# Kernel tuning notes

Hardware: AMD Instinct MI355X
Metric: run time of the kernel (lower is better)

Reference implementation:

```python
import jax, jax.numpy as jnp
import numpy as np

BLOCK = 32
A16_QMAX = 32767.0  # symmetric 16-bit activation fake-quant
W4_QMAX = 7.0       # symmetric 4-bit per-block weight fake-quant (LPBQ)
EPS = 1e-12


def qdq_a16_per_tensor(x):
    # per-tensor symmetric 16-bit fake quantize / dequantize
    scale = jnp.maximum(jnp.max(jnp.abs(x)) / A16_QMAX, EPS)
    return jnp.clip(jnp.round(x / scale), -A16_QMAX - 1.0, A16_QMAX) * scale


def qdq_weight_lpbq(w):
    # w: [out, in]; block-size-32 groups along the input dim, int4 symmetric
    o, i = w.shape
    wb = w.reshape(o, i // BLOCK, BLOCK)
    scale = jnp.maximum(jnp.max(jnp.abs(wb), axis=-1, keepdims=True) / W4_QMAX, EPS)
    q = jnp.clip(jnp.round(wb / scale), -W4_QMAX - 1.0, W4_QMAX) * scale
    return q.reshape(o, i)


def setup_inputs() -> dict:
    key = jax.random.key(0)
    k0, k1, k2, k3 = jax.random.split(key, 4)
    T, H, I = 4096, 2048, 6144  # tokens, hidden, intermediate
    x = jax.random.normal(k0, (T, H), dtype=jnp.float32)
    w_gate = jax.random.normal(k1, (I, H), dtype=jnp.float32) * 0.02
    w_up = jax.random.normal(k2, (I, H), dtype=jnp.float32) * 0.02
    w_down = jax.random.normal(k3, (H, I), dtype=jnp.float32) * 0.02
    return {"x": x, "w_gate": w_gate, "w_up": w_up, "w_down": w_down}


def reference(x, w_gate, w_up, w_down):
    x = qdq_a16_per_tensor(x)
    up = qdq_a16_per_tensor(x @ qdq_weight_lpbq(w_up).T)      # [T, I]
    gate = qdq_a16_per_tensor(x @ qdq_weight_lpbq(w_gate).T)  # [T, I]
    act = qdq_a16_per_tensor(jax.nn.silu(up))                  # SiLU on up branch (as in source)
    mid = qdq_a16_per_tensor(gate * act)
    return mid @ qdq_weight_lpbq(w_down).T                     # [T, H]
```

## Files before the change

kernel.cpp:

```cpp
#include <hip/hip_runtime.h>

#define T_DIM 4096
#define H_DIM 2048
#define I_DIM 6144

#define BM 128
#define BN 128
#define BK 64

typedef __bf16 bf16x8 __attribute__((ext_vector_type(8)));
typedef float f32x4 __attribute__((ext_vector_type(4)));

__device__ __forceinline__ unsigned short f2bf(float f) {
  unsigned u = __float_as_uint(f);
  u += 0x7FFFu + ((u >> 16) & 1u);
  return (unsigned short)(u >> 16);
}
__device__ __forceinline__ float bf2f(unsigned short h) {
  return __uint_as_float(((unsigned)h) << 16);
}

__device__ __forceinline__ void async16(const unsigned short* g, unsigned short* l) {
  __builtin_amdgcn_global_load_lds(
      (__attribute__((address_space(1))) void*)g,
      (__attribute__((address_space(3))) void*)l, 16, 0, 0);
}

__device__ __forceinline__ void qdq_w_one(const float* __restrict__ w,
                                          unsigned short* __restrict__ out, int i) {
  float4 v = ((const float4*)w)[i];
  float m = fmaxf(fmaxf(fabsf(v.x), fabsf(v.y)), fmaxf(fabsf(v.z), fabsf(v.w)));
  m = fmaxf(m, __shfl_xor(m, 1));
  m = fmaxf(m, __shfl_xor(m, 2));
  m = fmaxf(m, __shfl_xor(m, 4));
  const float s = fmaxf(m * (1.0f / 7.0f), 1e-12f);
  const float inv = 1.0f / s;
  ushort4 o;
  o.x = f2bf(fminf(fmaxf(rintf(v.x * inv), -8.f), 7.f) * s);
  o.y = f2bf(fminf(fmaxf(rintf(v.y * inv), -8.f), 7.f) * s);
  o.z = f2bf(fminf(fmaxf(rintf(v.z * inv), -8.f), 7.f) * s);
  o.w = f2bf(fminf(fmaxf(rintf(v.w * inv), -8.f), 7.f) * s);
  ((ushort4*)out)[i] = o;
}

__global__ void k_prep(const float* __restrict__ x, unsigned short* __restrict__ xq,
                       const float* __restrict__ w0, unsigned short* __restrict__ o0,
                       const float* __restrict__ w1, unsigned short* __restrict__ o1,
                       const float* __restrict__ w2, unsigned short* __restrict__ o2,
                       int nx4, int nw4) {
  const int i = blockIdx.x * blockDim.x + threadIdx.x;
  if (i < nx4) {
    float4 v = ((const float4*)x)[i];
    ushort4 o;
    o.x = f2bf(v.x); o.y = f2bf(v.y); o.z = f2bf(v.z); o.w = f2bf(v.w);
    ((ushort4*)xq)[i] = o;
  } else if (i < nx4 + nw4) {
    qdq_w_one(w0, o0, i - nx4);
  } else if (i < nx4 + 2 * nw4) {
    qdq_w_one(w1, o1, i - nx4 - nw4);
  } else {
    qdq_w_one(w2, o2, i - nx4 - 2 * nw4);
  }
}

template <int LDK>
__device__ __forceinline__ void gemm_core(const unsigned short* __restrict__ A,
                                          const unsigned short* __restrict__ B,
                                          unsigned short* ldsA, unsigned short* ldsB,
                                          long m0, long n0, int tid, f32x4 acc[4][4]) {
  const int lane = tid & 63;
  const int wv = tid >> 6;
  const int wm = (wv >> 1) << 6;
  const int wn = (wv & 1) << 6;
  const int quad = lane >> 4;
  const int l16 = lane & 15;
  const int sw = (l16 & 7);

  for (int k0 = 0; k0 < LDK; k0 += BK) {
    __syncthreads();
#pragma unroll
    for (int r = 0; r < 4; ++r) {
      const int c = r * 256 + tid;
      const int row = c >> 3;
      const int colc = ((c & 7) ^ (row & 7)) * 8;
      async16(A + (m0 + row) * LDK + k0 + colc, ldsA + (size_t)c * 8);
      async16(B + (n0 + row) * LDK + k0 + colc, ldsB + (size_t)c * 8);
    }
    __syncthreads();

#pragma unroll
    for (int ks = 0; ks < BK / 32; ++ks) {
      bf16x8 af[4], bfr[4];
      const int sj = ((ks * 4 + quad) ^ sw) * 8;
#pragma unroll
      for (int i = 0; i < 4; ++i) {
        af[i] = *(const bf16x8*)(ldsA + (wm + i * 16 + l16) * BK + sj);
        bfr[i] = *(const bf16x8*)(ldsB + (wn + i * 16 + l16) * BK + sj);
      }
#pragma unroll
      for (int i = 0; i < 4; ++i)
#pragma unroll
        for (int j = 0; j < 4; ++j)
          acc[i][j] = __builtin_amdgcn_mfma_f32_16x16x32_bf16(af[i], bfr[j], acc[i][j], 0, 0, 0);
    }
  }
}

__launch_bounds__(512)
__global__ void k_gemm_ug_fused(const unsigned short* __restrict__ xq,
                                const unsigned short* __restrict__ wu,
                                const unsigned short* __restrict__ wg,
                                unsigned short* __restrict__ mid) {
  __shared__ unsigned short lds[3 * BM * BK];
  const int tid = threadIdx.x;
  const int lane = tid & 63;
  const int wv = tid >> 6;
  const int half = wv >> 2;
  const int wq = wv & 3;
  const int wm = (wq >> 1) << 6;
  const int wn = (wq & 1) << 6;
  const int quad = lane >> 4;
  const int l16 = lane & 15;
  const int sw = (l16 & 7);
  const long m0 = (long)blockIdx.y * BM;
  const long n0 = (long)blockIdx.x * BN;
  unsigned short* ldsB = lds + (size_t)(1 + half) * BM * BK;

  f32x4 acc[4][4] = {};

  for (int k0 = 0; k0 < H_DIM; k0 += BK) {
    __syncthreads();
#pragma unroll
    for (int r = 0; r < 6; ++r) {
      const int idx = r * 512 + tid;
      const int t = idx >> 10;
      const int c = idx & 1023;
      const int row = c >> 3;
      const int colc = ((c & 7) ^ (row & 7)) * 8;
      const unsigned short* src =
          (t == 0) ? xq + (m0 + row) * H_DIM + k0 + colc
        : (t == 1) ? wu + (n0 + row) * H_DIM + k0 + colc
                   : wg + (n0 + row) * H_DIM + k0 + colc;
      async16(src, lds + (size_t)t * (BM * BK) + (size_t)c * 8);
    }
    __syncthreads();

#pragma unroll
    for (int ks = 0; ks < BK / 32; ++ks) {
      bf16x8 af[4], bfr[4];
      const int sj = ((ks * 4 + quad) ^ sw) * 8;
#pragma unroll
      for (int i = 0; i < 4; ++i) {
        af[i] = *(const bf16x8*)(lds + (wm + i * 16 + l16) * BK + sj);
        bfr[i] = *(const bf16x8*)(ldsB + (wn + i * 16 + l16) * BK + sj);
      }
#pragma unroll
      for (int i = 0; i < 4; ++i)
#pragma unroll
        for (int j = 0; j < 4; ++j)
          acc[i][j] = __builtin_amdgcn_mfma_f32_16x16x32_bf16(af[i], bfr[j], acc[i][j], 0, 0, 0);
    }
  }

  __syncthreads();
  const int rbase = wm + (quad << 2);
  const int cbase = wn + l16;
  if (half) {
#pragma unroll
    for (int i = 0; i < 4; ++i)
#pragma unroll
      for (int r = 0; r < 4; ++r) {
        const int row = rbase + i * 16 + r;
        const int swz = ((row >> 2) & 3) << 4;
#pragma unroll
        for (int j = 0; j < 4; ++j) {
          const int col = cbase + j * 16;
          lds[row * 128 + (col ^ swz)] = f2bf(acc[i][j][r]);
        }
      }
  }
  __syncthreads();
  if (!half) {
#pragma unroll
    for (int i = 0; i < 4; ++i)
#pragma unroll
      for (int r = 0; r < 4; ++r) {
        const int row = rbase + i * 16 + r;
        const int swz = ((row >> 2) & 3) << 4;
        const long grow = m0 + row;
#pragma unroll
        for (int j = 0; j < 4; ++j) {
          const int col = cbase + j * 16;
          const float u = acc[i][j][r];
          const float g = bf2f(lds[row * 128 + (col ^ swz)]);
          const float a = u * __frcp_rn(1.0f + __expf(-u));
          mid[grow * (long)I_DIM + n0 + col] = f2bf(a * g);
        }
      }
  }
}

__launch_bounds__(256)
__global__ void k_gemm_down(const unsigned short* __restrict__ A,
                            const unsigned short* __restrict__ B,
                            float* __restrict__ C) {
  __shared__ unsigned short lds[(BM + BN) * BK];
  const int tid = threadIdx.x;
  const long m0 = (long)blockIdx.y * BM;
  const long n0 = (long)blockIdx.x * BN;

  f32x4 acc[4][4] = {};
  gemm_core<I_DIM>(A, B, lds, lds + BM * BK, m0, n0, tid, acc);

  const int lane = tid & 63;
  const int wv = tid >> 6;
  const int wm = (wv >> 1) << 6;
  const int wn = (wv & 1) << 6;
  const int quad = lane >> 4;
  const int l16 = lane & 15;
  const long rbase = m0 + wm + (quad << 2);
  const long cbase = n0 + wn + l16;
#pragma unroll
  for (int i = 0; i < 4; ++i)
#pragma unroll
    for (int r = 0; r < 4; ++r) {
      const long grow = rbase + i * 16 + r;
#pragma unroll
      for (int j = 0; j < 4; ++j)
        C[grow * (long)H_DIM + cbase + j * 16] = acc[i][j][r];
    }
}

extern "C" void kernel_launch(void* const* d_in, const int* in_sizes, int n_in,
                              void* d_out, int out_size, void* d_ws, size_t ws_size,
                              hipStream_t stream) {
  (void)in_sizes; (void)n_in; (void)out_size; (void)ws_size;
  const float* x      = (const float*)d_in[0];
  const float* w_gate = (const float*)d_in[1];
  const float* w_up   = (const float*)d_in[2];
  const float* w_down = (const float*)d_in[3];

  char* ws = (char*)d_ws;
  const size_t OFF_XQ = 0;
  const size_t OFF_WU = OFF_XQ + (size_t)T_DIM * H_DIM * 2;
  const size_t OFF_WD = OFF_WU + (size_t)I_DIM * H_DIM * 2;
  const size_t OFF_MID = OFF_WD + (size_t)I_DIM * H_DIM * 2;
  unsigned short* xq  = (unsigned short*)(ws + OFF_XQ);
  unsigned short* wuq = (unsigned short*)(ws + OFF_WU);
  unsigned short* wdq = (unsigned short*)(ws + OFF_WD);
  unsigned short* mid = (unsigned short*)(ws + OFF_MID);
  unsigned short* wgq = (unsigned short*)d_out;

  const int nx4 = T_DIM * H_DIM / 4;
  const int nw4 = I_DIM * H_DIM / 4;

  k_prep<<<(nx4 + 3 * nw4) / 256, 256, 0, stream>>>(x, xq, w_up, wuq, w_gate, wgq,
                                                    w_down, wdq, nx4, nw4);

  k_gemm_ug_fused<<<dim3(I_DIM / BN, T_DIM / BM), 512, 0, stream>>>(xq, wuq, wgq, mid);

  k_gemm_down<<<dim3(H_DIM / BN, T_DIM / BM), 256, 0, stream>>>(mid, wdq, (float*)d_out);
}
```

Measured before the change: 503.5 us.

## Double-buffer LDS in both GEMMs and widen down-proj tile to 128x256

Both the fused up/gate GEMM and the down-projection GEMM now use two LDS buffers. The async global-to-LDS load for the next K slice is issued before computing on the current one, which removes one barrier per iteration and overlaps memory traffic with MFMA work. The down GEMM also moves to 512 threads with a 128x256 tile, which raises reuse of the A operand and halves its grid. The cost is doubled LDS use: 96KB for the fused kernel and 96KB for the down kernel, which likely limits occupancy to one block per CU. The down GEMM grid drops to 256 blocks.

```diff
diff --git a/kernel.cpp b/kernel.cpp
--- a/kernel.cpp
+++ b/kernel.cpp
@@ -7,6 +7,7 @@
 #define BM 128
 #define BN 128
 #define BK 64
+#define DBN 256
 
 typedef __bf16 bf16x8 __attribute__((ext_vector_type(8)));
 typedef float f32x4 __attribute__((ext_vector_type(4)));
@@ -63,55 +64,12 @@
   }
 }
 
-template <int LDK>
-__device__ __forceinline__ void gemm_core(const unsigned short* __restrict__ A,
-                                          const unsigned short* __restrict__ B,
-                                          unsigned short* ldsA, unsigned short* ldsB,
-                                          long m0, long n0, int tid, f32x4 acc[4][4]) {
-  const int lane = tid & 63;
-  const int wv = tid >> 6;
-  const int wm = (wv >> 1) << 6;
-  const int wn = (wv & 1) << 6;
-  const int quad = lane >> 4;
-  const int l16 = lane & 15;
-  const int sw = (l16 & 7);
-
-  for (int k0 = 0; k0 < LDK; k0 += BK) {
-    __syncthreads();
-#pragma unroll
-    for (int r = 0; r < 4; ++r) {
-      const int c = r * 256 + tid;
-      const int row = c >> 3;
-      const int colc = ((c & 7) ^ (row & 7)) * 8;
-      async16(A + (m0 + row) * LDK + k0 + colc, ldsA + (size_t)c * 8);
-      async16(B + (n0 + row) * LDK + k0 + colc, ldsB + (size_t)c * 8);
-    }
-    __syncthreads();
-
-#pragma unroll
-    for (int ks = 0; ks < BK / 32; ++ks) {
-      bf16x8 af[4], bfr[4];
-      const int sj = ((ks * 4 + quad) ^ sw) * 8;
-#pragma unroll
-      for (int i = 0; i < 4; ++i) {
-        af[i] = *(const bf16x8*)(ldsA + (wm + i * 16 + l16) * BK + sj);
-        bfr[i] = *(const bf16x8*)(ldsB + (wn + i * 16 + l16) * BK + sj);
-      }
-#pragma unroll
-      for (int i = 0; i < 4; ++i)
-#pragma unroll
-        for (int j = 0; j < 4; ++j)
-          acc[i][j] = __builtin_amdgcn_mfma_f32_16x16x32_bf16(af[i], bfr[j], acc[i][j], 0, 0, 0);
-    }
-  }
-}
-
 __launch_bounds__(512)
 __global__ void k_gemm_ug_fused(const unsigned short* __restrict__ xq,
                                 const unsigned short* __restrict__ wu,
                                 const unsigned short* __restrict__ wg,
                                 unsigned short* __restrict__ mid) {
-  __shared__ unsigned short lds[3 * BM * BK];
+  __shared__ unsigned short lds[2 * 3 * BM * BK];
   const int tid = threadIdx.x;
   const int lane = tid & 63;
   const int wv = tid >> 6;
@@ -124,35 +82,36 @@
   const int sw = (l16 & 7);
   const long m0 = (long)blockIdx.y * BM;
   const long n0 = (long)blockIdx.x * BN;
-  unsigned short* ldsB = lds + (size_t)(1 + half) * BM * BK;
 
   f32x4 acc[4][4] = {};
 
-  for (int k0 = 0; k0 < H_DIM; k0 += BK) {
-    __syncthreads();
+  auto stage = [&](int buf, int k0) {
+    unsigned short* base = lds + (size_t)buf * (3 * BM * BK);
 #pragma unroll
     for (int r = 0; r < 6; ++r) {
       const int idx = r * 512 + tid;
-      const int t = idx >> 10;
+      const int tt = idx >> 10;
       const int c = idx & 1023;
       const int row = c >> 3;
       const int colc = ((c & 7) ^ (row & 7)) * 8;
       const unsigned short* src =
-          (t == 0) ? xq + (m0 + row) * H_DIM + k0 + colc
-        : (t == 1) ? wu + (n0 + row) * H_DIM + k0 + colc
-                   : wg + (n0 + row) * H_DIM + k0 + colc;
-      async16(src, lds + (size_t)t * (BM * BK) + (size_t)c * 8);
-    }
-    __syncthreads();
-
+          (tt == 0) ? xq + (m0 + row) * H_DIM + k0 + colc
+        : (tt == 1) ? wu + (n0 + row) * H_DIM + k0 + colc
+                    : wg + (n0 + row) * H_DIM + k0 + colc;
+      async16(src, base + (size_t)tt * (BM * BK) + (size_t)c * 8);
+    }
+  };
+  auto compute = [&](int buf) {
+    const unsigned short* bA = lds + (size_t)buf * (3 * BM * BK);
+    const unsigned short* bB = bA + (size_t)(1 + half) * (BM * BK);
 #pragma unroll
     for (int ks = 0; ks < BK / 32; ++ks) {
       bf16x8 af[4], bfr[4];
       const int sj = ((ks * 4 + quad) ^ sw) * 8;
 #pragma unroll
       for (int i = 0; i < 4; ++i) {
-        af[i] = *(const bf16x8*)(lds + (wm + i * 16 + l16) * BK + sj);
-        bfr[i] = *(const bf16x8*)(ldsB + (wn + i * 16 + l16) * BK + sj);
+        af[i] = *(const bf16x8*)(bA + (wm + i * 16 + l16) * BK + sj);
+        bfr[i] = *(const bf16x8*)(bB + (wn + i * 16 + l16) * BK + sj);
       }
 #pragma unroll
       for (int i = 0; i < 4; ++i)
@@ -160,7 +119,18 @@
         for (int j = 0; j < 4; ++j)
           acc[i][j] = __builtin_amdgcn_mfma_f32_16x16x32_bf16(af[i], bfr[j], acc[i][j], 0, 0, 0);
     }
-  }
+  };
+
+  stage(0, 0);
+  __syncthreads();
+  int cur = 0;
+  for (int k0 = BK; k0 < H_DIM; k0 += BK) {
+    stage(cur ^ 1, k0);
+    compute(cur);
+    __syncthreads();
+    cur ^= 1;
+  }
+  compute(cur);
 
   __syncthreads();
   const int rbase = wm + (quad << 2);
@@ -200,24 +170,73 @@
   }
 }
 
-__launch_bounds__(256)
+__launch_bounds__(512)
 __global__ void k_gemm_down(const unsigned short* __restrict__ A,
                             const unsigned short* __restrict__ B,
                             float* __restrict__ C) {
-  __shared__ unsigned short lds[(BM + BN) * BK];
+  __shared__ unsigned short lds[2 * (BM + DBN) * BK];
   const int tid = threadIdx.x;
-  const long m0 = (long)blockIdx.y * BM;
-  const long n0 = (long)blockIdx.x * BN;
-
-  f32x4 acc[4][4] = {};
-  gemm_core<I_DIM>(A, B, lds, lds + BM * BK, m0, n0, tid, acc);
-
   const int lane = tid & 63;
   const int wv = tid >> 6;
-  const int wm = (wv >> 1) << 6;
-  const int wn = (wv & 1) << 6;
+  const int wm = (wv >> 2) << 6;
+  const int wn = (wv & 3) << 6;
   const int quad = lane >> 4;
   const int l16 = lane & 15;
+  const int sw = (l16 & 7);
+  const long m0 = (long)blockIdx.y * BM;
+  const long n0 = (long)blockIdx.x * DBN;
+
+  f32x4 acc[4][4] = {};
+
+  auto stage = [&](int buf, int k0) {
+    unsigned short* base = lds + (size_t)buf * ((BM + DBN) * BK);
+#pragma unroll
+    for (int r = 0; r < 6; ++r) {
+      const int idx = r * 512 + tid;
+      if (idx < 1024) {
+        const int row = idx >> 3;
+        const int colc = ((idx & 7) ^ (row & 7)) * 8;
+        async16(A + (m0 + row) * I_DIM + k0 + colc, base + (size_t)idx * 8);
+      } else {
+        const int c = idx - 1024;
+        const int row = c >> 3;
+        const int colc = ((c & 7) ^ (row & 7)) * 8;
+        async16(B + (n0 + row) * I_DIM + k0 + colc,
+                base + (size_t)(BM * BK) + (size_t)c * 8);
+      }
+    }
+  };
+  auto compute = [&](int buf) {
+    const unsigned short* bA = lds + (size_t)buf * ((BM + DBN) * BK);
+    const unsigned short* bB = bA + BM * BK;
+#pragma unroll
+    for (int ks = 0; ks < BK / 32; ++ks) {
+      bf16x8 af[4], bfr[4];
+      const int sj = ((ks * 4 + quad) ^ sw) * 8;
+#pragma unroll
+      for (int i = 0; i < 4; ++i) {
+        af[i] = *(const bf16x8*)(bA + (wm + i * 16 + l16) * BK + sj);
+        bfr[i] = *(const bf16x8*)(bB + (wn + i * 16 + l16) * BK + sj);
+      }
+#pragma unroll
+      for (int i = 0; i < 4; ++i)
+#pragma unroll
+        for (int j = 0; j < 4; ++j)
+          acc[i][j] = __builtin_amdgcn_mfma_f32_16x16x32_bf16(af[i], bfr[j], acc[i][j], 0, 0, 0);
+    }
+  };
+
+  stage(0, 0);
+  __syncthreads();
+  int cur = 0;
+  for (int k0 = BK; k0 < I_DIM; k0 += BK) {
+    stage(cur ^ 1, k0);
+    compute(cur);
+    __syncthreads();
+    cur ^= 1;
+  }
+  compute(cur);
+
   const long rbase = m0 + wm + (quad << 2);
   const long cbase = n0 + wn + l16;
 #pragma unroll
@@ -259,5 +278,5 @@
 
   k_gemm_ug_fused<<<dim3(I_DIM / BN, T_DIM / BM), 512, 0, stream>>>(xq, wuq, wgq, mid);
 
-  k_gemm_down<<<dim3(H_DIM / BN, T_DIM / BM), 256, 0, stream>>>(mid, wdq, (float*)d_out);
-}
+  k_gemm_down<<<dim3(H_DIM / DBN, T_DIM / BM), 512, 0, stream>>>(mid, wdq, (float*)d_out);
+}
```

Result: no change. 510.3 us (+1.4%).
